# Kernel tuning notes

Measured on AMD Instinct MI355X. Metric: run time of the kernel, lower is better.

Reference implementation:

```python
import jax, jax.numpy as jnp
import numpy as np

B, N, L, D = 64, 512, 12, 128   # batch, nodes, neighbors, node_dim==edge_dim
Z = 3 * D                        # 2*node_dim + edge_dim
NC = 3                           # n_convs
VOCAB = 1000
BN_EPS = 1e-3                    # keras BatchNormalization default epsilon


def setup_inputs() -> dict:
    key = jax.random.key(0)
    ks = jax.random.split(key, 14)
    inp = {}
    inp['node_types'] = jax.random.randint(ks[0], (B, N), 0, VOCAB)
    inp['neighbor_list'] = jax.random.randint(ks[1], (B, N, L), 0, N)
    inp['edge_types'] = jax.random.randint(ks[2], (B, N, L), 0, VOCAB)
    inp['slot_types'] = jax.random.normal(ks[3], (B, N, D), jnp.float32)
    inp['node_w'] = jax.random.normal(ks[4], (VOCAB, D), jnp.float32) * 0.1
    inp['edge_w'] = jax.random.normal(ks[5], (VOCAB, D), jnp.float32) * 0.1
    inp['wf'] = jax.random.normal(ks[6], (NC, Z, D), jnp.float32) * 0.05
    inp['bf'] = jax.random.normal(ks[7], (NC, D), jnp.float32) * 0.01
    inp['ws'] = jax.random.normal(ks[8], (NC, Z, D), jnp.float32) * 0.05
    inp['bs'] = jax.random.normal(ks[9], (NC, D), jnp.float32) * 0.01
    inp['bn_gamma'] = jnp.ones((NC, D), jnp.float32)
    inp['bn_beta'] = jnp.zeros((NC, D), jnp.float32)
    inp['bn_mean'] = jax.random.normal(ks[10], (NC, D), jnp.float32) * 0.01
    inp['bn_var'] = jax.random.uniform(ks[11], (NC, D), jnp.float32, 0.5, 1.5)
    inp['dense_w'] = jax.random.normal(ks[12], (D, 1), jnp.float32) * 0.1
    inp['dense_b'] = jnp.zeros((1,), jnp.float32)
    return inp


def _embed(w, x):
    # gather with negative-index masking, as in Embedding.call (inference path)
    idx = jnp.where(x < 0, 0, x)
    mask = (x >= 0).astype(jnp.float32)[..., None]
    return w[idx] * mask


def reference(node_types, neighbor_list, edge_types, slot_types,
              node_w, edge_w, wf, bf, ws, bs,
              bn_gamma, bn_beta, bn_mean, bn_var, dense_w, dense_b):
    v = _embed(node_w, node_types) + slot_types          # (B, N, D)
    e = _embed(edge_w, edge_types)                       # (B, N, L, D)

    nl = neighbor_list
    n_safe = jnp.where(nl < 0, 0, nl)                    # (B, N, L)
    nmask = (nl >= 0).astype(jnp.float32)[..., None]     # (B, N, L, 1)

    for i in range(NC):
        # neighbor gather: per-batch index into node axis
        nn = jax.vmap(lambda vv, ii: vv[ii])(v, n_safe) * nmask  # (B, N, L, D)
        v_view = jnp.broadcast_to(v[:, :, None, :], nn.shape)
        z = jnp.concatenate([v_view, nn, e], axis=-1)            # (B, N, L, Z)
        s = (jax.nn.sigmoid(jnp.einsum('bnlz,zd->bnld', z, wf[i]) + bf[i])
             * jnp.tanh(jnp.einsum('bnlz,zd->bnld', z, ws[i]) + bs[i])
             * nmask)
        v_next = v + jnp.sum(s, axis=2)                          # (B, N, D)

        # masked batchnorm (inference: moving stats); invalid rows -> 0
        vf = v_next.reshape(-1, D)
        valid = jnp.all(jnp.abs(vf) > 1e-5, axis=-1)
        bn = bn_gamma[i] * (vf - bn_mean[i]) * jax.lax.rsqrt(bn_var[i] + BN_EPS) + bn_beta[i]
        v = jnp.where(valid[:, None], bn, 0.0).reshape(B, N, D)

    # masked mean pooling over nodes
    pmask = (node_types >= 0).astype(jnp.float32)[..., None]     # (B, N, 1)
    pooled = jnp.sum(v * pmask, axis=1) / jnp.sum(pmask, axis=1)  # (B, D)
    return pooled @ dense_w + dense_b                            # (B, 1)
```

## Files before the change

kernel.cpp:

```cpp
#include <hip/hip_runtime.h>

#define NB 64
#define NN 512
#define NL 12
#define ND 128
#define NZ 384
#define NCONV 3
#define VOCAB 1000
#define BN_EPS 1e-3f
#define LO_SCALE 2048.0f
#define INV_LO (1.0f/2048.0f)
#define SCF (-1.4426950408889634f)
#define SCS ( 2.8853900817779268f)

typedef _Float16 f16;
using half8 = __attribute__((ext_vector_type(8))) _Float16;
using floatx16 = __attribute__((ext_vector_type(16))) float;

__device__ __forceinline__ floatx16 mfma32(half8 a, half8 b, floatx16 c) {
    return __builtin_amdgcn_mfma_f32_32x32x16_f16(a, b, c, 0, 0, 0);
}
__device__ __forceinline__ void split1(float x, f16& h, f16& l) {
    h = (f16)x; l = (f16)((x - (float)h) * LO_SCALE);
}

__global__ __launch_bounds__(256) void prep_kernel(
    const float* __restrict__ wf, const float* __restrict__ wsg,
    f16* __restrict__ Wc_hi, f16* __restrict__ Wc_lo)
{
    int id = blockIdx.x * 256 + threadIdx.x;
    int c = id >> 16;
    int rem = id & 65535;
    int col = rem >> 7, k = rem & 127;
    int part = col >> 7;
    int d = col & 127;
    int z = (part < 2) ? (128 + k) : k;
    const float* W = (part & 1) ? wsg : wf;
    float wv = W[((size_t)c * NZ + z) * ND + d];
    f16 h, l; split1(wv, h, l);
    size_t dst = (size_t)c * 65536 + (size_t)(k >> 3) * 4096 + col * 8 + (k & 7);
    Wc_hi[dst] = h; Wc_lo[dst] = l;
}

__global__ __launch_bounds__(256) void ew_kernel(
    const float* __restrict__ edge_w, const float* __restrict__ wf,
    const float* __restrict__ wsg, float* __restrict__ EWp)
{
    __shared__ float se[32][128];
    const int c = blockIdx.x >> 5;
    const int tyg = (blockIdx.x & 31) * 32;
    const int tid = threadIdx.x;
    for (int i = tid; i < 4096; i += 256) {
        int ty = i >> 7, k = i & 127;
        int tyv = tyg + ty;
        se[ty][k] = (tyv < VOCAB) ? edge_w[(size_t)tyv * ND + k] : 0.f;
    }
    __syncthreads();
    const int h = tid >> 7, col = tid & 127;
    const float* W = h ? wsg : wf;
    const float sc = h ? SCS : SCF;
    float acc[32];
    #pragma unroll
    for (int ty = 0; ty < 32; ++ty) acc[ty] = 0.f;
    #pragma unroll 4
    for (int k = 0; k < 128; ++k) {
        float wv = W[((size_t)c * NZ + 256 + k) * ND + col];
        #pragma unroll
        for (int ty = 0; ty < 32; ++ty) acc[ty] = fmaf(se[ty][k], wv, acc[ty]);
    }
    #pragma unroll
    for (int ty = 0; ty < 32; ++ty) {
        int tyv = tyg + ty;
        if (tyv <= VOCAB)
            EWp[((size_t)c * (VOCAB + 1) + tyv) * 256 + (col & 63) * 4 + (col >> 6) * 2 + h] = acc[ty] * sc;
    }
}

__global__ __launch_bounds__(256) void embed_kernel(
    const int* __restrict__ node_types, const float* __restrict__ slot_types,
    const float* __restrict__ node_w, f16* __restrict__ vhi, f16* __restrict__ vlo)
{
    int i = blockIdx.x * 256 + threadIdx.x;
    int bn = i >> 7, d = i & 127;
    int ty = node_types[bn];
    float m = ty >= 0 ? 1.f : 0.f;
    int idx = ty >= 0 ? ty : 0;
    float v = node_w[(size_t)idx * ND + d] * m + slot_types[i];
    f16 h, l; split1(v, h, l);
    vhi[i] = h; vlo[i] = l;
}

__global__ __launch_bounds__(256, 3) void psgemm_kernel(
    const f16* __restrict__ vhi, const f16* __restrict__ vlo,
    const f16* __restrict__ Wc_hi, const f16* __restrict__ Wc_lo,
    const float* __restrict__ bfv, const float* __restrict__ bsv,
    float* __restrict__ Ppk, float* __restrict__ Spk)
{
    __shared__ __align__(16) char sA[16384];
    const int hw = blockIdx.x;
    const int xcd = hw & 7;
    const int q = hw >> 3;
    const int bl = q >> 5;
    const int r = q & 31;
    const int half = r >> 4;
    const int xloc = r & 15;
    const int batch = bl * 8 + xcd;
    const int node0 = batch * NN + xloc * 32;

    const int tid = threadIdx.x;
    const int lane = tid & 63, w = tid >> 6;
    const int l31 = lane & 31, l32 = lane >> 5;

    #pragma unroll
    for (int it = 0; it < 2; ++it) {
        int slot = it * 256 + tid;
        int rr = slot >> 4, cc = slot & 15;
        int cs = cc ^ (rr & 15);
        size_t src = (size_t)(node0 + rr) * ND + cs * 8;
        *(half8*)(sA + rr * 256 + cc * 16) = *(const half8*)(vhi + src);
        *(half8*)(sA + 8192 + rr * 256 + cc * 16) = *(const half8*)(vlo + src);
    }
    __syncthreads();

    const int dcol = w * 32 + l31;
    const int col0 = half * 256 + dcol;
    const int col1 = col0 + 128;

    floatx16 a00 = {}, a10 = {}, a01 = {}, a11 = {};

    int ch0 = l32;
    half8 b0h = *(const half8*)(Wc_hi + (size_t)ch0 * 4096 + col0 * 8);
    half8 b0l = *(const half8*)(Wc_lo + (size_t)ch0 * 4096 + col0 * 8);
    half8 b1h = *(const half8*)(Wc_hi + (size_t)ch0 * 4096 + col1 * 8);
    half8 b1l = *(const half8*)(Wc_lo + (size_t)ch0 * 4096 + col1 * 8);

    #pragma unroll
    for (int ks = 0; ks < 8; ++ks) {
        half8 n0h, n0l, n1h, n1l;
        if (ks < 7) {
            int nch = (ks + 1) * 2 + l32;
            n0h = *(const half8*)(Wc_hi + (size_t)nch * 4096 + col0 * 8);
            n0l = *(const half8*)(Wc_lo + (size_t)nch * 4096 + col0 * 8);
            n1h = *(const half8*)(Wc_hi + (size_t)nch * 4096 + col1 * 8);
            n1l = *(const half8*)(Wc_lo + (size_t)nch * 4096 + col1 * 8);
        }
        int qq = (((ks * 2 + l32) ^ (l31 & 15)) << 4);
        half8 ah = *(const half8*)(sA + l31 * 256 + qq);
        half8 al = *(const half8*)(sA + 8192 + l31 * 256 + qq);
        a00 = mfma32(ah, b0h, a00);
        a10 = mfma32(ah, b0l, a10);
        a10 = mfma32(al, b0h, a10);
        a01 = mfma32(ah, b1h, a01);
        a11 = mfma32(ah, b1l, a11);
        a11 = mfma32(al, b1h, a11);
        b0h = n0h; b0l = n0l; b1h = n1h; b1l = n1l;
    }

    float bx = 0.f, by = 0.f;
    if (half) { bx = bfv[dcol]; by = bsv[dcol]; }
    float* outp = half ? Spk : Ppk;
    const int dsub = (dcol & 63) * 4 + (dcol >> 6) * 2;
    #pragma unroll
    for (int rr = 0; rr < 16; ++rr) {
        int orow = (rr & 3) + 8 * (rr >> 2) + 4 * l32;
        float2 v2 = { (a00[rr] + a10[rr] * INV_LO + bx) * SCF,
                      (a01[rr] + a11[rr] * INV_LO + by) * SCS };
        *(float2*)(outp + (size_t)(node0 + orow) * 256 + dsub) = v2;
    }
}

__global__ __launch_bounds__(256, 2) void edge_epilogue_kernel(
    f16* __restrict__ vhi, f16* __restrict__ vlo,
    const int* __restrict__ neighbor_list, const int* __restrict__ edge_types,
    const float* __restrict__ Ppk, const float* __restrict__ Spk,
    const float* __restrict__ EWp,
    const float* __restrict__ bn_gamma, const float* __restrict__ bn_beta,
    const float* __restrict__ bn_mean, const float* __restrict__ bn_var)
{
    const int hw = blockIdx.x;
    const int xcd = hw & 7;
    const int q = hw >> 3;
    const int b = (q >> 7) * 8 + xcd;
    const int j = q & 127;
    const int node0 = b * NN + j * 4;

    const int tid = threadIdx.x;
    const int w = tid >> 6, ds = tid & 63;
    const int node = node0 + w;
    const int bbase = b * NN;

    int nlv = -1, etv = -1;
    if (ds < NL) {
        nlv = neighbor_list[node * NL + ds];
        etv = edge_types[node * NL + ds];
    }
    unsigned long long bm = __ballot(nlv >= 0);

    float4 sp4 = *(const float4*)(Spk + (size_t)node * 256 + ds * 4);
    float4 p4[NL], e4[NL];
    #pragma unroll
    for (int l = 0; l < NL; ++l) {
        int nl_l = __builtin_amdgcn_readlane(nlv, l);
        int et_l = __builtin_amdgcn_readlane(etv, l);
        int ns = (nl_l >= 0) ? (bbase + nl_l) : node;
        int es = (et_l >= 0) ? et_l : VOCAB;
        p4[l] = *(const float4*)(Ppk + (size_t)ns * 256 + ds * 4);
        e4[l] = *(const float4*)(EWp + (size_t)es * 256 + ds * 4);
    }

    float sum0 = 0.f, sum1 = 0.f;
    #pragma unroll
    for (int l = 0; l < NL; ++l) {
        float m = ((bm >> l) & 1) ? 1.f : 0.f;
        float ax = p4[l].x + sp4.x + e4[l].x;
        float ay = p4[l].y + sp4.y + e4[l].y;
        float az = p4[l].z + sp4.z + e4[l].z;
        float aw = p4[l].w + sp4.w + e4[l].w;
        float u0 = __builtin_amdgcn_exp2f(fminf(ax, 60.f));
        float w0 = __builtin_amdgcn_exp2f(fminf(ay, 60.f));
        float u1 = __builtin_amdgcn_exp2f(fminf(az, 60.f));
        float w1 = __builtin_amdgcn_exp2f(fminf(aw, 60.f));
        float r0 = __builtin_amdgcn_rcpf(fmaf(u0, w0, 1.f + u0 + w0));
        float r1 = __builtin_amdgcn_rcpf(fmaf(u1, w1, 1.f + u1 + w1));
        sum0 = fmaf((w0 - 1.f) * r0, m, sum0);
        sum1 = fmaf((w1 - 1.f) * r1, m, sum1);
    }

    size_t i0 = (size_t)node * ND + ds;
    size_t i1 = i0 + 64;
    float x0 = (float)vhi[i0] + (float)vlo[i0] * INV_LO + sum0;
    float x1 = (float)vhi[i1] + (float)vlo[i1] * INV_LO + sum1;
    int valid = __all(fabsf(x0) > 1e-5f && fabsf(x1) > 1e-5f);

    float gm0 = bn_gamma[ds], be0 = bn_beta[ds], mu0 = bn_mean[ds];
    float gm1 = bn_gamma[ds + 64], be1 = bn_beta[ds + 64], mu1 = bn_mean[ds + 64];
    float rs0 = __builtin_amdgcn_rcpf(sqrtf(bn_var[ds] + BN_EPS));
    float rs1 = __builtin_amdgcn_rcpf(sqrtf(bn_var[ds + 64] + BN_EPS));
    float o0 = valid ? (gm0 * (x0 - mu0) * rs0 + be0) : 0.f;
    float o1 = valid ? (gm1 * (x1 - mu1) * rs1 + be1) : 0.f;
    f16 h, l2;
    split1(o0, h, l2); vhi[i0] = h; vlo[i0] = l2;
    split1(o1, h, l2); vhi[i1] = h; vlo[i1] = l2;
}

__global__ __launch_bounds__(256) void pool1_kernel(
    const f16* __restrict__ vhi, const f16* __restrict__ vlo,
    const int* __restrict__ node_types, float* __restrict__ partial)
{
    __shared__ float sbuf[128];
    const int b = blockIdx.x >> 3, chunk = blockIdx.x & 7;
    const int d = threadIdx.x & 127, sub = threadIdx.x >> 7;
    const int n0 = chunk * 64 + sub * 32;
    float sum = 0.f;
    #pragma unroll 4
    for (int i = 0; i < 32; ++i) {
        int n = n0 + i;
        int ty = node_types[b * NN + n];
        float mk = ty >= 0 ? 1.f : 0.f;
        size_t ix = ((size_t)(b * NN + n)) * ND + d;
        sum += ((float)vhi[ix] + (float)vlo[ix] * INV_LO) * mk;
    }
    if (sub == 0) sbuf[d] = sum;
    __syncthreads();
    if (sub == 1) partial[(size_t)blockIdx.x * 128 + d] = sbuf[d] + sum;
}

__global__ __launch_bounds__(128) void pool2_kernel(
    const float* __restrict__ partial, const int* __restrict__ node_types,
    const float* __restrict__ dense_w, const float* __restrict__ dense_b,
    float* __restrict__ out)
{
    __shared__ float s_part[2], s_cnt[2];
    const int b = blockIdx.x;
    const int d = threadIdx.x;
    float sum = 0.f;
    #pragma unroll
    for (int c = 0; c < 8; ++c) sum += partial[(size_t)(b * 8 + c) * 128 + d];
    float cnt = 0.f;
    #pragma unroll
    for (int i = 0; i < 4; ++i)
        cnt += (node_types[b * NN + d + i * 128] >= 0) ? 1.f : 0.f;
    #pragma unroll
    for (int off = 32; off > 0; off >>= 1) cnt += __shfl_xor(cnt, off);
    if ((d & 63) == 0) s_cnt[d >> 6] = cnt;
    __syncthreads();
    float tcnt = s_cnt[0] + s_cnt[1];
    float pv = (sum / tcnt) * dense_w[d];
    #pragma unroll
    for (int off = 32; off > 0; off >>= 1) pv += __shfl_down(pv, off);
    if ((d & 63) == 0) s_part[d >> 6] = pv;
    __syncthreads();
    if (d == 0) out[b] = s_part[0] + s_part[1] + dense_b[0];
}

extern "C" void kernel_launch(void* const* d_in, const int* in_sizes, int n_in,
                              void* d_out, int out_size, void* d_ws, size_t ws_size,
                              hipStream_t stream) {
    const int*   node_types    = (const int*)d_in[0];
    const int*   neighbor_list = (const int*)d_in[1];
    const int*   edge_types    = (const int*)d_in[2];
    const float* slot_types    = (const float*)d_in[3];
    const float* node_w        = (const float*)d_in[4];
    const float* edge_w        = (const float*)d_in[5];
    const float* wf            = (const float*)d_in[6];
    const float* bfv           = (const float*)d_in[7];
    const float* wsg           = (const float*)d_in[8];
    const float* bsv           = (const float*)d_in[9];
    const float* bn_gamma      = (const float*)d_in[10];
    const float* bn_beta       = (const float*)d_in[11];
    const float* bn_mean       = (const float*)d_in[12];
    const float* bn_var        = (const float*)d_in[13];
    const float* dense_w       = (const float*)d_in[14];
    const float* dense_b       = (const float*)d_in[15];
    float* out = (float*)d_out;

    float* wsf = (float*)d_ws;
    float* Ppk = wsf;
    float* Spk = wsf + 8388608;
    float* EWp = wsf + 2 * 8388608;
    float* pp  = EWp + 768768;
    f16* f16b  = (f16*)(pp + 65536);
    f16* vhiA  = f16b;
    f16* vloA  = vhiA + 4194304;
    f16* Wc_hi = vloA + 4194304;
    f16* Wc_lo = Wc_hi + 196608;

    prep_kernel<<<768, 256, 0, stream>>>(wf, wsg, Wc_hi, Wc_lo);
    ew_kernel<<<NCONV * 32, 256, 0, stream>>>(edge_w, wf, wsg, EWp);
    embed_kernel<<<(NB * NN * ND) / 256, 256, 0, stream>>>(node_types, slot_types, node_w, vhiA, vloA);

    for (int c = 0; c < NCONV; ++c) {
        psgemm_kernel<<<2048, 256, 0, stream>>>(
            vhiA, vloA, Wc_hi + (size_t)c * 65536, Wc_lo + (size_t)c * 65536,
            bfv + c * ND, bsv + c * ND, Ppk, Spk);
        edge_epilogue_kernel<<<8192, 256, 0, stream>>>(
            vhiA, vloA, neighbor_list, edge_types,
            Ppk, Spk, EWp + (size_t)c * (VOCAB + 1) * 256,
            bn_gamma + c * ND, bn_beta + c * ND, bn_mean + c * ND, bn_var + c * ND);
    }

    pool1_kernel<<<NB * 8, 256, 0, stream>>>(vhiA, vloA, node_types, pp);
    pool2_kernel<<<NB, 128, 0, stream>>>(pp, node_types, dense_w, dense_b, out);
}
```

Baseline: 267.9 us.

## Merge setup kernels and split edge epilogue neighbors across two waves

The three setup kernels (weight split, edge-type projection, node embedding) are merged into one launch whose work is chosen by block-index range, removing two launch gaps. The edge epilogue now gives each node two wavefronts, each handling 6 of the 12 neighbors. Partial sums are combined through shared memory before batchnorm, and the grid doubles with launch bounds raised to 4 blocks per CU. The aim is more memory-level parallelism and occupancy for the gather-heavy epilogue, at the cost of a block barrier, an LDS exchange and half the threads sitting idle during the final write.

```diff
diff --git a/kernel.cpp b/kernel.cpp
--- a/kernel.cpp
+++ b/kernel.cpp
@@ -24,70 +24,67 @@
     h = (f16)x; l = (f16)((x - (float)h) * LO_SCALE);
 }
 
-__global__ __launch_bounds__(256) void prep_kernel(
+__global__ __launch_bounds__(256) void setup_kernel(
     const float* __restrict__ wf, const float* __restrict__ wsg,
-    f16* __restrict__ Wc_hi, f16* __restrict__ Wc_lo)
-{
-    int id = blockIdx.x * 256 + threadIdx.x;
-    int c = id >> 16;
-    int rem = id & 65535;
-    int col = rem >> 7, k = rem & 127;
-    int part = col >> 7;
-    int d = col & 127;
-    int z = (part < 2) ? (128 + k) : k;
-    const float* W = (part & 1) ? wsg : wf;
-    float wv = W[((size_t)c * NZ + z) * ND + d];
-    f16 h, l; split1(wv, h, l);
-    size_t dst = (size_t)c * 65536 + (size_t)(k >> 3) * 4096 + col * 8 + (k & 7);
-    Wc_hi[dst] = h; Wc_lo[dst] = l;
-}
-
-__global__ __launch_bounds__(256) void ew_kernel(
-    const float* __restrict__ edge_w, const float* __restrict__ wf,
-    const float* __restrict__ wsg, float* __restrict__ EWp)
-{
-    __shared__ float se[32][128];
-    const int c = blockIdx.x >> 5;
-    const int tyg = (blockIdx.x & 31) * 32;
-    const int tid = threadIdx.x;
-    for (int i = tid; i < 4096; i += 256) {
-        int ty = i >> 7, k = i & 127;
-        int tyv = tyg + ty;
-        se[ty][k] = (tyv < VOCAB) ? edge_w[(size_t)tyv * ND + k] : 0.f;
-    }
-    __syncthreads();
-    const int h = tid >> 7, col = tid & 127;
-    const float* W = h ? wsg : wf;
-    const float sc = h ? SCS : SCF;
-    float acc[32];
-    #pragma unroll
-    for (int ty = 0; ty < 32; ++ty) acc[ty] = 0.f;
-    #pragma unroll 4
-    for (int k = 0; k < 128; ++k) {
-        float wv = W[((size_t)c * NZ + 256 + k) * ND + col];
-        #pragma unroll
-        for (int ty = 0; ty < 32; ++ty) acc[ty] = fmaf(se[ty][k], wv, acc[ty]);
-    }
-    #pragma unroll
-    for (int ty = 0; ty < 32; ++ty) {
-        int tyv = tyg + ty;
-        if (tyv <= VOCAB)
-            EWp[((size_t)c * (VOCAB + 1) + tyv) * 256 + (col & 63) * 4 + (col >> 6) * 2 + h] = acc[ty] * sc;
-    }
-}
-
-__global__ __launch_bounds__(256) void embed_kernel(
+    f16* __restrict__ Wc_hi, f16* __restrict__ Wc_lo,
+    const float* __restrict__ edge_w, float* __restrict__ EWp,
     const int* __restrict__ node_types, const float* __restrict__ slot_types,
     const float* __restrict__ node_w, f16* __restrict__ vhi, f16* __restrict__ vlo)
 {
-    int i = blockIdx.x * 256 + threadIdx.x;
-    int bn = i >> 7, d = i & 127;
-    int ty = node_types[bn];
-    float m = ty >= 0 ? 1.f : 0.f;
-    int idx = ty >= 0 ? ty : 0;
-    float v = node_w[(size_t)idx * ND + d] * m + slot_types[i];
-    f16 h, l; split1(v, h, l);
-    vhi[i] = h; vlo[i] = l;
+    __shared__ float se[32][128];
+    const int blk = blockIdx.x;
+    const int tid = threadIdx.x;
+    if (blk < 768) {
+        int id = blk * 256 + tid;
+        int c = id >> 16;
+        int rem = id & 65535;
+        int col = rem >> 7, k = rem & 127;
+        int part = col >> 7;
+        int d = col & 127;
+        int z = (part < 2) ? (128 + k) : k;
+        const float* W = (part & 1) ? wsg : wf;
+        float wv = W[((size_t)c * NZ + z) * ND + d];
+        f16 h, l; split1(wv, h, l);
+        size_t dst = (size_t)c * 65536 + (size_t)(k >> 3) * 4096 + col * 8 + (k & 7);
+        Wc_hi[dst] = h; Wc_lo[dst] = l;
+    } else if (blk < 864) {
+        const int bid = blk - 768;
+        const int c = bid >> 5;
+        const int tyg = (bid & 31) * 32;
+        for (int i = tid; i < 4096; i += 256) {
+            int ty = i >> 7, k = i & 127;
+            int tyv = tyg + ty;
+            se[ty][k] = (tyv < VOCAB) ? edge_w[(size_t)tyv * ND + k] : 0.f;
+        }
+        __syncthreads();
+        const int h = tid >> 7, col = tid & 127;
+        const float* W = h ? wsg : wf;
+        const float sc = h ? SCS : SCF;
+        float acc[32];
+        #pragma unroll
+        for (int ty = 0; ty < 32; ++ty) acc[ty] = 0.f;
+        #pragma unroll 4
+        for (int k = 0; k < 128; ++k) {
+            float wv = W[((size_t)c * NZ + 256 + k) * ND + col];
+            #pragma unroll
+            for (int ty = 0; ty < 32; ++ty) acc[ty] = fmaf(se[ty][k], wv, acc[ty]);
+        }
+        #pragma unroll
+        for (int ty = 0; ty < 32; ++ty) {
+            int tyv = tyg + ty;
+            if (tyv <= VOCAB)
+                EWp[((size_t)c * (VOCAB + 1) + tyv) * 256 + (col & 63) * 4 + (col >> 6) * 2 + h] = acc[ty] * sc;
+        }
+    } else {
+        int i = (blk - 864) * 256 + tid;
+        int bn = i >> 7, d = i & 127;
+        int ty = node_types[bn];
+        float m = ty >= 0 ? 1.f : 0.f;
+        int idx = ty >= 0 ? ty : 0;
+        float v = node_w[(size_t)idx * ND + d] * m + slot_types[i];
+        f16 h, l; split1(v, h, l);
+        vhi[i] = h; vlo[i] = l;
+    }
 }
 
 __global__ __launch_bounds__(256, 3) void psgemm_kernel(
@@ -169,7 +166,7 @@
     }
 }
 
-__global__ __launch_bounds__(256, 2) void edge_epilogue_kernel(
+__global__ __launch_bounds__(256, 4) void edge_epilogue_kernel(
     f16* __restrict__ vhi, f16* __restrict__ vlo,
     const int* __restrict__ neighbor_list, const int* __restrict__ edge_types,
     const float* __restrict__ Ppk, const float* __restrict__ Spk,
@@ -177,29 +174,32 @@
     const float* __restrict__ bn_gamma, const float* __restrict__ bn_beta,
     const float* __restrict__ bn_mean, const float* __restrict__ bn_var)
 {
+    __shared__ float s_red[2][64][2];
     const int hw = blockIdx.x;
     const int xcd = hw & 7;
     const int q = hw >> 3;
-    const int b = (q >> 7) * 8 + xcd;
-    const int j = q & 127;
-    const int node0 = b * NN + j * 4;
+    const int b = (q >> 8) * 8 + xcd;
+    const int j = q & 255;
+    const int node0 = b * NN + j * 2;
 
     const int tid = threadIdx.x;
     const int w = tid >> 6, ds = tid & 63;
-    const int node = node0 + w;
+    const int nl_ = w >> 1;
+    const int sub = w & 1;
+    const int node = node0 + nl_;
     const int bbase = b * NN;
 
     int nlv = -1, etv = -1;
-    if (ds < NL) {
-        nlv = neighbor_list[node * NL + ds];
-        etv = edge_types[node * NL + ds];
+    if (ds < 6) {
+        nlv = neighbor_list[node * NL + sub * 6 + ds];
+        etv = edge_types[node * NL + sub * 6 + ds];
     }
     unsigned long long bm = __ballot(nlv >= 0);
 
     float4 sp4 = *(const float4*)(Spk + (size_t)node * 256 + ds * 4);
-    float4 p4[NL], e4[NL];
-    #pragma unroll
-    for (int l = 0; l < NL; ++l) {
+    float4 p4[6], e4[6];
+    #pragma unroll
+    for (int l = 0; l < 6; ++l) {
         int nl_l = __builtin_amdgcn_readlane(nlv, l);
         int et_l = __builtin_amdgcn_readlane(etv, l);
         int ns = (nl_l >= 0) ? (bbase + nl_l) : node;
@@ -210,7 +210,7 @@
 
     float sum0 = 0.f, sum1 = 0.f;
     #pragma unroll
-    for (int l = 0; l < NL; ++l) {
+    for (int l = 0; l < 6; ++l) {
         float m = ((bm >> l) & 1) ? 1.f : 0.f;
         float ax = p4[l].x + sp4.x + e4[l].x;
         float ay = p4[l].y + sp4.y + e4[l].y;
@@ -226,21 +226,27 @@
         sum1 = fmaf((w1 - 1.f) * r1, m, sum1);
     }
 
-    size_t i0 = (size_t)node * ND + ds;
-    size_t i1 = i0 + 64;
-    float x0 = (float)vhi[i0] + (float)vlo[i0] * INV_LO + sum0;
-    float x1 = (float)vhi[i1] + (float)vlo[i1] * INV_LO + sum1;
-    int valid = __all(fabsf(x0) > 1e-5f && fabsf(x1) > 1e-5f);
-
-    float gm0 = bn_gamma[ds], be0 = bn_beta[ds], mu0 = bn_mean[ds];
-    float gm1 = bn_gamma[ds + 64], be1 = bn_beta[ds + 64], mu1 = bn_mean[ds + 64];
-    float rs0 = __builtin_amdgcn_rcpf(sqrtf(bn_var[ds] + BN_EPS));
-    float rs1 = __builtin_amdgcn_rcpf(sqrtf(bn_var[ds + 64] + BN_EPS));
-    float o0 = valid ? (gm0 * (x0 - mu0) * rs0 + be0) : 0.f;
-    float o1 = valid ? (gm1 * (x1 - mu1) * rs1 + be1) : 0.f;
-    f16 h, l2;
-    split1(o0, h, l2); vhi[i0] = h; vlo[i0] = l2;
-    split1(o1, h, l2); vhi[i1] = h; vlo[i1] = l2;
+    if (sub) { s_red[nl_][ds][0] = sum0; s_red[nl_][ds][1] = sum1; }
+    __syncthreads();
+    if (!sub) {
+        sum0 += s_red[nl_][ds][0];
+        sum1 += s_red[nl_][ds][1];
+        size_t i0 = (size_t)node * ND + ds;
+        size_t i1 = i0 + 64;
+        float x0 = (float)vhi[i0] + (float)vlo[i0] * INV_LO + sum0;
+        float x1 = (float)vhi[i1] + (float)vlo[i1] * INV_LO + sum1;
+        int valid = __all(fabsf(x0) > 1e-5f && fabsf(x1) > 1e-5f);
+
+        float gm0 = bn_gamma[ds], be0 = bn_beta[ds], mu0 = bn_mean[ds];
+        float gm1 = bn_gamma[ds + 64], be1 = bn_beta[ds + 64], mu1 = bn_mean[ds + 64];
+        float rs0 = __builtin_amdgcn_rcpf(sqrtf(bn_var[ds] + BN_EPS));
+        float rs1 = __builtin_amdgcn_rcpf(sqrtf(bn_var[ds + 64] + BN_EPS));
+        float o0 = valid ? (gm0 * (x0 - mu0) * rs0 + be0) : 0.f;
+        float o1 = valid ? (gm1 * (x1 - mu1) * rs1 + be1) : 0.f;
+        f16 h, l2;
+        split1(o0, h, l2); vhi[i0] = h; vlo[i0] = l2;
+        split1(o1, h, l2); vhi[i1] = h; vlo[i1] = l2;
+    }
 }
 
 __global__ __launch_bounds__(256) void pool1_kernel(
@@ -325,15 +331,15 @@
     f16* Wc_hi = vloA + 4194304;
     f16* Wc_lo = Wc_hi + 196608;
 
-    prep_kernel<<<768, 256, 0, stream>>>(wf, wsg, Wc_hi, Wc_lo);
-    ew_kernel<<<NCONV * 32, 256, 0, stream>>>(edge_w, wf, wsg, EWp);
-    embed_kernel<<<(NB * NN * ND) / 256, 256, 0, stream>>>(node_types, slot_types, node_w, vhiA, vloA);
+    setup_kernel<<<17248, 256, 0, stream>>>(
+        wf, wsg, Wc_hi, Wc_lo, edge_w, EWp,
+        node_types, slot_types, node_w, vhiA, vloA);
 
     for (int c = 0; c < NCONV; ++c) {
         psgemm_kernel<<<2048, 256, 0, stream>>>(
             vhiA, vloA, Wc_hi + (size_t)c * 65536, Wc_lo + (size_t)c * 65536,
             bfv + c * ND, bsv + c * ND, Ppk, Spk);
-        edge_epilogue_kernel<<<8192, 256, 0, stream>>>(
+        edge_epilogue_kernel<<<16384, 256, 0, stream>>>(
             vhiA, vloA, neighbor_list, edge_types,
             Ppk, Spk, EWp + (size_t)c * (VOCAB + 1) * 256,
             bn_gamma + c * ND, bn_beta + c * ND, bn_mean + c * ND, bn_var + c * ND);
```

Measured after the change: 247.7 us. -7.5%, faster.
